# Optimization experiments

Hardware: AMD Instinct MI355X
Metric: run time of the kernel (lower is better)

## Reference

```python
import jax, jax.numpy as jnp
import numpy as np

# Scattering config (matches init_kwargs)
J, L, MAX_ORDER = 3, 8, 2
H = W = 128
LEN_COEFF = 1 + J * L + L * L * (J * (J - 1) // 2)  # 217
B = 16
N_OUT = 6


def _gabor_2d(M, N, sigma, theta, xi, slant):
    """Periodized 2D Gabor centered at (0,0), kymatio convention."""
    R = np.array([[np.cos(theta), -np.sin(theta)], [np.sin(theta), np.cos(theta)]])
    D = np.array([[1.0, 0.0], [0.0, slant * slant]])
    curv = R @ D @ R.T / (2.0 * sigma * sigma)
    gab = np.zeros((M, N), np.complex128)
    for ex in range(-2, 3):
        for ey in range(-2, 3):
            xx, yy = np.mgrid[ex * M:(ex + 1) * M, ey * N:(ey + 1) * N]
            arg = -(curv[0, 0] * xx * xx + (curv[0, 1] + curv[1, 0]) * xx * yy
                    + curv[1, 1] * yy * yy) \
                  + 1j * xi * (xx * np.cos(theta) + yy * np.sin(theta))
            gab += np.exp(arg)
    return gab / (2.0 * np.pi * sigma * sigma / slant)


def _morlet_2d(M, N, sigma, theta, xi, slant):
    wv = _gabor_2d(M, N, sigma, theta, xi, slant)
    g = _gabor_2d(M, N, sigma, theta, 0.0, slant)
    K = wv.sum() / g.sum()  # zero-mean correction
    return wv - K * g


def _filter_bank(M, N, J_, L_):
    psi = np.zeros((J_, L_, M, N), np.complex64)
    for j in range(J_):
        sigma = 0.8 * 2.0 ** j
        xi = 3.0 / 4.0 * np.pi / 2.0 ** j
        for l in range(L_):
            theta = (int(L_ - L_ / 2 - 1) - l) * np.pi / L_
            psi[j, l] = np.fft.fft2(
                _morlet_2d(M, N, sigma, theta, xi, 4.0 / L_)).astype(np.complex64)
    phi = np.fft.fft2(
        _gabor_2d(M, N, 0.8 * 2.0 ** (J_ - 1), 0.0, 0.0, 1.0)).astype(np.complex64)
    return jnp.asarray(phi), jnp.asarray(psi)


def setup_inputs() -> dict:
    key = jax.random.key(0)
    k1, k2, k3 = jax.random.split(key, 3)
    x = jax.random.normal(k1, (B, H, W), dtype=jnp.float32)
    weight = jax.random.normal(k2, (N_OUT, LEN_COEFF), dtype=jnp.float32) / np.sqrt(LEN_COEFF)
    bias = jax.random.normal(k3, (N_OUT,), dtype=jnp.float32) * 0.01
    phi_f, psi_f = _filter_bank(H, W, J, L)
    return {"x": x, "weight": weight, "bias": bias, "phi_f": phi_f, "psi_f": psi_f}


def _scattering(x, phi_f, psi_f):
    # x: (B,H,W); phi_f: (H,W) complex; psi_f: (J,L,H,W) complex (Fourier-domain)
    k = 2 ** J
    xf = jnp.fft.fft2(x)
    # Order 0: low-pass then subsample by 2^J (exact spatial subsample of band-limited conv)
    outs = [jnp.fft.ifft2(xf * phi_f).real[:, None, ::k, ::k]]  # (B,1,h,w)
    U1 = []
    for j1 in range(J):
        u1 = jnp.abs(jnp.fft.ifft2(xf[:, None] * psi_f[j1]))  # (B,L,H,W)
        U1.append(u1)
        outs.append(jnp.fft.ifft2(jnp.fft.fft2(u1) * phi_f).real[..., ::k, ::k])
    if MAX_ORDER >= 2:
        for j1 in range(J):
            u1f = jnp.fft.fft2(U1[j1])  # (B,L,H,W)
            for j2 in range(j1 + 1, J):
                u2 = jnp.abs(jnp.fft.ifft2(u1f[:, :, None] * psi_f[j2]))  # (B,L,L,H,W)
                s2 = jnp.fft.ifft2(jnp.fft.fft2(u2) * phi_f).real[..., ::k, ::k]
                outs.append(s2.reshape(s2.shape[0], L * L, H // k, W // k))
    return jnp.concatenate(outs, axis=1)  # (B, LEN_COEFF, h, w)


def reference(x, weight, bias, phi_f, psi_f):
    coeffs = _scattering(x, phi_f, psi_f)            # (B, 217, 16, 16)
    coeffs_spav = coeffs.mean(axis=(-2, -1))         # spatial average -> (B, 217)
    out = coeffs_spav @ weight.T + bias              # Linear(217 -> 6)
    return out                                       # Identity output activation
```

## Files before the change

kernel.cpp:

```cpp
#include <hip/hip_runtime.h>
#include <math.h>


#define HW 128
#define NPIX 16384
#define NCOEFF 217
#define NB 16
#define NOUT 6
#define NT 1024
#define NBLK2 3072
#define PI_F 3.14159265358979f
#define CMAX_EPS 1e-6f

__device__ float  g_w8[64];
__device__ float  g_psi[24 * NPIX];
__device__ float  g_cmax[24 * 128];
__device__ float  g_coeffs[NB * NCOEFF];
__device__ unsigned g_ticket;
__device__ float2 g_xf[NB * NPIX];
__device__ float  g_u1[NB * 16 * NPIX];
__device__ float2 g_u1f[NB * 16 * NPIX];

#if defined(__has_builtin)
#  if __has_builtin(__builtin_amdgcn_permlane32_swap)
#    define USE_PL32 1
#  else
#    define USE_PL32 0
#  endif
#  if __has_builtin(__builtin_amdgcn_permlane16_swap)
#    define USE_PL16 1
#  else
#    define USE_PL16 0
#  endif
#else
#  define USE_PL32 0
#  define USE_PL16 0
#endif

__device__ __forceinline__ float2 cmul2(float2 a, float2 b) {
  return make_float2(a.x*b.x - a.y*b.y, a.x*b.y + a.y*b.x);
}
__device__ __forceinline__ float2 cmulc2(float2 a, float2 b) {
  return make_float2(a.x*b.x + a.y*b.y, a.y*b.x - a.x*b.y);
}
__device__ __forceinline__ float fsqrt_fast(float x) {
  return __builtin_amdgcn_sqrtf(x);
}

template <int S>
__device__ __forceinline__ float shx(float v) {
  if constexpr (S == 1)
    return __int_as_float(__builtin_amdgcn_mov_dpp(
        __float_as_int(v), 0xB1, 0xF, 0xF, true));
  else if constexpr (S == 2)
    return __int_as_float(__builtin_amdgcn_mov_dpp(
        __float_as_int(v), 0x4E, 0xF, 0xF, true));
  else if constexpr (S == 4)
    return __int_as_float(__builtin_amdgcn_ds_swizzle(
        __float_as_int(v), 0x101F));
  else if constexpr (S == 8)
    return __int_as_float(__builtin_amdgcn_mov_dpp(
        __float_as_int(v), 0x128, 0xF, 0xF, true));
  else
    return __shfl_xor(v, S);
}

__device__ __forceinline__ float bft32(float v, float sg) {
#if USE_PL32
  auto r = __builtin_amdgcn_permlane32_swap(
      __float_as_int(v), __float_as_int(v), false, false);
  return fmaf(sg, __int_as_float(r[1]), __int_as_float(r[0]));
#else
  return fmaf(sg, v, __shfl_xor(v, 32));
#endif
}
__device__ __forceinline__ float bft16(float v, float sg) {
#if USE_PL16
  auto r = __builtin_amdgcn_permlane16_swap(
      __float_as_int(v), __float_as_int(v), false, false);
  return fmaf(sg, __int_as_float(r[1]), __int_as_float(r[0]));
#else
  return fmaf(sg, v, __shfl_xor(v, 16));
#endif
}

__device__ __forceinline__ float2 cndrot_n(float2 u, bool m) {
  return m ? make_float2(u.y, -u.x) : u;
}
__device__ __forceinline__ float2 cndrot_p(float2 u, bool m) {
  return m ? make_float2(-u.y, u.x) : u;
}

struct TwState {
  float2 tw0, wA, wB;
  float  sg[6];
  bool   rA, rB, rC;
};

__device__ __forceinline__ void make_tw(int lane, TwState &T) {
  float s, c;
  sincosf(-PI_F * (float)lane / 64.f, &s, &c);
  T.tw0 = make_float2(c, s);
  int kA = 2 * ((lane >> 4) & 1) + ((lane >> 5) & 1);
  sincosf(-PI_F * (float)((lane & 15) * kA) / 32.f, &s, &c);
  T.wA = make_float2(c, s);
  int kB = 2 * ((lane >> 2) & 1) + ((lane >> 3) & 1);
  sincosf(-PI_F * (float)((lane & 3) * kB) / 8.f, &s, &c);
  T.wB = make_float2(c, s);
#pragma unroll
  for (int k = 0; k < 6; ++k)
    T.sg[k] = (lane & (32 >> k)) ? -1.f : 1.f;
  T.rA = (lane & 48) == 48;
  T.rB = (lane & 12) == 12;
  T.rC = (lane & 3) == 3;
}

__device__ __forceinline__ float2 fwd_p32(float2 v, const TwState &T) {
  float2 u; u.x = bft32(v.x, T.sg[0]); u.y = bft32(v.y, T.sg[0]);
  u = cndrot_n(u, T.rA);
  float2 t; t.x = bft16(u.x, T.sg[1]); t.y = bft16(u.y, T.sg[1]);
  return cmul2(t, T.wA);
}
__device__ __forceinline__ float2 fwd_p8(float2 v, const TwState &T) {
  float2 u; u.x = fmaf(T.sg[2], v.x, shx<8>(v.x));
            u.y = fmaf(T.sg[2], v.y, shx<8>(v.y));
  u = cndrot_n(u, T.rB);
  float2 t; t.x = fmaf(T.sg[3], u.x, shx<4>(u.x));
            t.y = fmaf(T.sg[3], u.y, shx<4>(u.y));
  return cmul2(t, T.wB);
}
__device__ __forceinline__ float2 fwd_p2(float2 v, const TwState &T) {
  float2 u; u.x = fmaf(T.sg[4], v.x, shx<2>(v.x));
            u.y = fmaf(T.sg[4], v.y, shx<2>(v.y));
  u = cndrot_n(u, T.rC);
  float2 t; t.x = fmaf(T.sg[5], u.x, shx<1>(u.x));
            t.y = fmaf(T.sg[5], u.y, shx<1>(u.y));
  return t;
}
__device__ __forceinline__ float2 inv_p1(float2 v, const TwState &T) {
  float2 u; u.x = fmaf(T.sg[5], v.x, shx<1>(v.x));
            u.y = fmaf(T.sg[5], v.y, shx<1>(v.y));
  u = cndrot_p(u, T.rC);
  float2 t; t.x = fmaf(T.sg[4], u.x, shx<2>(u.x));
            t.y = fmaf(T.sg[4], u.y, shx<2>(u.y));
  return t;
}
__device__ __forceinline__ float2 inv_p4(float2 v, const TwState &T) {
  float2 m = cmulc2(v, T.wB);
  float2 u; u.x = fmaf(T.sg[3], m.x, shx<4>(m.x));
            u.y = fmaf(T.sg[3], m.y, shx<4>(m.y));
  u = cndrot_p(u, T.rB);
  float2 t; t.x = fmaf(T.sg[2], u.x, shx<8>(u.x));
            t.y = fmaf(T.sg[2], u.y, shx<8>(u.y));
  return t;
}
__device__ __forceinline__ float2 inv_p16(float2 v, const TwState &T) {
  float2 m = cmulc2(v, T.wA);
  float2 u; u.x = bft16(m.x, T.sg[1]); u.y = bft16(m.y, T.sg[1]);
  u = cndrot_p(u, T.rA);
  float2 t; t.x = bft32(u.x, T.sg[0]); t.y = bft32(u.y, T.sg[0]);
  return t;
}

__device__ __forceinline__ void fft128_fwd(float2 &a, float2 &b, const TwState &T) {
  float2 t = make_float2(a.x - b.x, a.y - b.y);
  a = make_float2(a.x + b.x, a.y + b.y);
  b = cmul2(t, T.tw0);
  a = fwd_p32(a, T); b = fwd_p32(b, T);
  a = fwd_p8(a, T);  b = fwd_p8(b, T);
  a = fwd_p2(a, T);  b = fwd_p2(b, T);
}

__device__ __forceinline__ void fft128_inv(float2 &a, float2 &b, const TwState &T) {
  a = inv_p1(a, T);  b = inv_p1(b, T);
  a = inv_p4(a, T);  b = inv_p4(b, T);
  a = inv_p16(a, T); b = inv_p16(b, T);
  float2 t = cmulc2(b, T.tw0);
  float2 na = make_float2(a.x + t.x, a.y + t.y);
  b = make_float2(a.x - t.x, a.y - t.y);
  a = na;
}

__device__ __forceinline__ int fmap(int p) {
  int l = p & 63, t = p >> 6;
  int br = (int)(__brev((unsigned)l) >> 26);
  return 2 * br + t;
}

__device__ __forceinline__ void fparams(int f, float &sig, float &xi, float &co, float &si) {
  int j = f >> 3, l = f & 7;
  sig = 0.8f * (float)(1 << j);
  xi = 0.75f * PI_F / (float)(1 << j);
  float th = (float)(3 - l) * PI_F / 8.f;
  sincosf(th, &si, &co);
}

__device__ __forceinline__ float gab_hat_fast(float tr, float tc, float sig,
                                              float xi, float co, float si, int j) {
  float hs = 0.5f * sig * sig;
  int m1lo, m1hi, m2lo, m2hi;
  if (j == 0)      { m1lo = -1; m1hi = 1; m2lo = -1; m2hi = 1; }
  else if (j == 1) { m1lo = -1; m1hi = 0; m2lo = -1; m2hi = 0; }
  else {
    m1lo = (tr > 0.5f) ? -1 : 0; m1hi = m1lo;
    m2lo = (tc > 0.5f) ? -1 : 0; m2hi = m2lo;
  }
  float acc = 0.f;
  for (int m1 = m1lo; m1 <= m1hi; ++m1)
    for (int m2 = m2lo; m2 <= m2hi; ++m2) {
      float w1 = 2.f * PI_F * (tr + (float)m1) - xi * co;
      float w2 = 2.f * PI_F * (tc + (float)m2) - xi * si;
      float a1 = co * w1 + si * w2;
      float a2 = -si * w1 + co * w2;
      acc += __expf(-hs * (a1 * a1 + 4.f * a2 * a2));
    }
  return acc;
}

__device__ __forceinline__ float ct8(int k) {
  k &= 7;
  float m = (k & 1) ? 0.70710678118654752f : ((k & 2) ? 0.f : 1.f);
  return (k >= 3 && k <= 5) ? -m : m;
}

__device__ __forceinline__ void transp(const float2 va[8], const float2 vb[8],
                                       float2 na[8], float2 nb[8],
                                       int w, int l, float2* buf) {
#pragma unroll
  for (int i = 0; i < 8; ++i) buf[(w + 16 * i) * 65 + l] = va[i];
  __syncthreads();
#pragma unroll
  for (int k = 0; k < 4; ++k) {
    na[k] = buf[l * 65 + 16 * k + w];
    nb[k] = buf[(l + 64) * 65 + 16 * k + w];
  }
  __syncthreads();
#pragma unroll
  for (int i = 0; i < 8; ++i) buf[(w + 16 * i) * 65 + l] = vb[i];
  __syncthreads();
#pragma unroll
  for (int k = 0; k < 4; ++k) {
    na[4 + k] = buf[l * 65 + 16 * k + w];
    nb[4 + k] = buf[(l + 64) * 65 + 16 * k + w];
  }
}

__global__ void __launch_bounds__(NT, 4)
k_prep(const float* __restrict__ x) {
  __shared__ float2 buf[128 * 65];
  __shared__ float red[16];
  __shared__ float w8s[64];
  __shared__ float sK[2];
  int tid = threadIdx.x, blk = blockIdx.x;
  if (blk >= NB) {
    if (blk == NB && tid == 0) g_ticket = 0;
    int idx = (blk - NB) * NT + tid;
    int f = idx >> 14;
    int q = idx & (NPIX - 1);
    int pc = q >> 7, pr = q & 127;
    float tr = (float)fmap(pr) / 128.f;
    float tc = (float)fmap(pc) / 128.f;
    float sig, xi, co, si;
    fparams(f, sig, xi, co, si);
    int j = f >> 3;
    float hsK = 0.5f * sig * sig;
    int wv = tid >> 6;
    if (wv < 2) {
      int t = tid & 63;
      float term = 0.f;
      if (t < 25) {
        int m1 = t / 5 - 2, m2 = t % 5 - 2;
        float xe = (wv == 0) ? xi : 0.f;
        float w1 = 2.f * PI_F * (float)m1 - xe * co;
        float w2 = 2.f * PI_F * (float)m2 - xe * si;
        float a1 = co * w1 + si * w2, a2 = -si * w1 + co * w2;
        term = expf(-hsK * (a1 * a1 + 4.f * a2 * a2));
      }
      for (int off = 32; off; off >>= 1) term += __shfl_xor(term, off);
      if (t == 0) sK[wv] = term;
    }
    __syncthreads();
    float Kf = sK[0] / sK[1];
    float p = gab_hat_fast(tr, tc, sig, xi, co, si, j)
            - Kf * gab_hat_fast(tr, tc, sig, 0.f, co, si, j);
    g_psi[idx] = p;
    float m = fabsf(p);
    for (int off = 32; off; off >>= 1) m = fmaxf(m, __shfl_xor(m, off));
    if ((tid & 63) == 0)
      atomicMax((unsigned int*)&g_cmax[idx >> 7], __float_as_uint(m));
    return;
  }
  int b = blk;
  int l = tid & 63, w = tid >> 6;
  if (tid < 64) {
    const float hs8 = 0.5f * 3.2f * 3.2f;
    float P[8];
#pragma unroll
    for (int K = 0; K < 8; ++K) {
      float acc = 0.f;
      for (int m = -2; m <= 2; ++m) {
        float wv = 2.f * PI_F * ((float)K / 8.f + (float)m);
        acc += expf(-hs8 * wv * wv);
      }
      P[K] = acc;
    }
    int r = tid >> 3, s = tid & 7;
    float acc = 0.f;
#pragma unroll
    for (int K1 = 0; K1 < 8; ++K1)
#pragma unroll
      for (int K2 = 0; K2 < 8; ++K2)
        acc += P[K1] * P[K2] * ct8(K1 * r + K2 * s);
    w8s[tid] = acc;
    g_w8[tid] = acc;
  }
  TwState T; make_tw(l, T);
  const float inv = 1.f / 16384.f;
  const float* xb = x + b * NPIX;
  float2 va[8], vb[8], na[8], nb[8];
  float sacc = 0.f;
#pragma unroll
  for (int i = 0; i < 8; ++i) {
    int r = w + 16 * i;
    float v0 = xb[r * HW + l], v1 = xb[r * HW + l + 64];
    va[i] = make_float2(v0, 0.f); vb[i] = make_float2(v1, 0.f);
    sacc += v0 + v1;
  }
  __syncthreads();
  float w8v = w8s[((w & 7) << 3) | (l & 7)];
  sacc *= w8v;
  for (int off = 32; off; off >>= 1) sacc += __shfl_xor(sacc, off);
  if (l == 0) red[w] = sacc;
#pragma unroll
  for (int i = 0; i < 8; ++i) fft128_fwd(va[i], vb[i], T);
  transp(va, vb, na, nb, w, l, buf);
#pragma unroll
  for (int j = 0; j < 8; ++j) fft128_fwd(na[j], nb[j], T);
  float2* o = g_xf + (size_t)b * NPIX;
#pragma unroll
  for (int j = 0; j < 8; ++j) {
    int c = w + 16 * j;
    o[c * HW + l] = na[j];
    o[c * HW + l + 64] = nb[j];
  }
  if (tid == 0) {
    float s = 0.f;
    for (int i = 0; i < 16; ++i) s += red[i];
    g_coeffs[b * NCOEFF + 0] = s * inv;
  }
}

__global__ void __launch_bounds__(NT, 4)
k_inv1() {
  __shared__ float2 buf[128 * 65];
  __shared__ float red[16];
  __shared__ float w8s[64];
  int tid = threadIdx.x, blk = blockIdx.x;
  int b = blk / 24, f = blk % 24;
  int l = tid & 63, w = tid >> 6;
  if (tid < 64) w8s[tid] = g_w8[tid];
  TwState T; make_tw(l, T);
  const float inv = 1.f / 16384.f;
  const float2* X = g_xf + (size_t)b * NPIX;
  const float*  P = g_psi + f * NPIX;
  float2 va[8], vb[8], na[8], nb[8];
  bool kp[8];
#pragma unroll
  for (int j = 0; j < 8; ++j) {
    int c = w + 16 * j;
    kp[j] = g_cmax[f * 128 + c] > CMAX_EPS;
    if (kp[j]) {
      float2 x0 = X[c * HW + l], x1 = X[c * HW + l + 64];
      float p0 = P[c * HW + l],  p1 = P[c * HW + l + 64];
      na[j] = make_float2(x0.x * p0, x0.y * p0);
      nb[j] = make_float2(x1.x * p1, x1.y * p1);
    } else {
      na[j] = make_float2(0.f, 0.f);
      nb[j] = make_float2(0.f, 0.f);
    }
  }
#pragma unroll
  for (int j = 0; j < 8; ++j) if (kp[j]) fft128_inv(na[j], nb[j], T);
  transp(na, nb, va, vb, w, l, buf);
#pragma unroll
  for (int i = 0; i < 8; ++i) fft128_inv(va[i], vb[i], T);
  float w8v = w8s[((w & 7) << 3) | (l & 7)];
  float s1 = 0.f;
  float u0a[8], u1a[8];
#pragma unroll
  for (int i = 0; i < 8; ++i) {
    u0a[i] = fsqrt_fast(va[i].x * va[i].x + va[i].y * va[i].y);
    u1a[i] = fsqrt_fast(vb[i].x * vb[i].x + vb[i].y * vb[i].y);
    s1 += u0a[i] + u1a[i];
  }
  s1 *= w8v;
  for (int off = 32; off; off >>= 1) s1 += __shfl_xor(s1, off);
  if (l == 0) red[w] = s1;
  __syncthreads();
  if (tid == 0) {
    float s = 0.f;
    for (int i = 0; i < 16; ++i) s += red[i];
    g_coeffs[b * NCOEFF + 1 + f] = s * (inv * inv);
  }
  if (f < 16) {
    float* o = g_u1 + (size_t)(b * 16 + f) * NPIX;
#pragma unroll
    for (int i = 0; i < 8; ++i) {
      int r = w + 16 * i;
      o[r * HW + l] = u0a[i];
      o[r * HW + l + 64] = u1a[i];
    }
  }
}

__global__ void __launch_bounds__(NT, 4)
k_fwd1() {
  __shared__ float2 buf[128 * 65];
  int tid = threadIdx.x, chan = blockIdx.x;
  int l = tid & 63, w = tid >> 6;
  TwState T; make_tw(l, T);
  const float* u = g_u1 + (size_t)chan * NPIX;
  float2 va[8], vb[8], na[8], nb[8];
#pragma unroll
  for (int i = 0; i < 8; ++i) {
    int r = w + 16 * i;
    va[i] = make_float2(u[r * HW + l], 0.f);
    vb[i] = make_float2(u[r * HW + l + 64], 0.f);
  }
#pragma unroll
  for (int i = 0; i < 8; ++i) fft128_fwd(va[i], vb[i], T);
  transp(va, vb, na, nb, w, l, buf);
#pragma unroll
  for (int j = 0; j < 8; ++j) fft128_fwd(na[j], nb[j], T);
  float2* o = g_u1f + (size_t)chan * NPIX;
#pragma unroll
  for (int j = 0; j < 8; ++j) {
    int c = w + 16 * j;
    o[c * HW + l] = na[j];
    o[c * HW + l + 64] = nb[j];
  }
}

__global__ void __launch_bounds__(NT, 4)
k_order2(const float* __restrict__ wgt, const float* __restrict__ bias,
         float* __restrict__ out) {
  __shared__ float2 buf[128 * 65];
  __shared__ float red[16];
  __shared__ float w8s[64];
  __shared__ unsigned sLast;
  int tid = threadIdx.x, blk = blockIdx.x;
  int b, pair, l1, l2, j1, j2;
  if (blk < 2048) {
    l1 = blk & 7;
    int t = blk >> 3;
    b = t >> 4;
    int cons = t & 15;
    pair = cons >> 3;
    j2 = 1 + pair;
    l2 = cons & 7;
    j1 = 0;
  } else {
    int rr = blk - 2048;
    l1 = rr & 7;
    int t = rr >> 3;
    b = t >> 3;
    l2 = t & 7;
    j1 = 1; j2 = 2; pair = 2;
  }
  int fi = j2 * 8 + l2;
  int l = tid & 63, w = tid >> 6;
  if (tid < 64) w8s[tid] = g_w8[tid];
  TwState T; make_tw(l, T);
  const float inv = 1.f / 16384.f;
  const float2* X = g_u1f + (size_t)(b * 16 + j1 * 8 + l1) * NPIX;
  const float*  P = g_psi + fi * NPIX;
  float2 va[8], vb[8], na[8], nb[8];
  bool kp[8];
#pragma unroll
  for (int j = 0; j < 8; ++j) {
    int c = w + 16 * j;
    kp[j] = g_cmax[fi * 128 + c] > CMAX_EPS;
    if (kp[j]) {
      float2 x0 = X[c * HW + l], x1 = X[c * HW + l + 64];
      float p0 = P[c * HW + l],  p1 = P[c * HW + l + 64];
      na[j] = make_float2(x0.x * p0, x0.y * p0);
      nb[j] = make_float2(x1.x * p1, x1.y * p1);
    } else {
      na[j] = make_float2(0.f, 0.f);
      nb[j] = make_float2(0.f, 0.f);
    }
  }
#pragma unroll
  for (int j = 0; j < 8; ++j) if (kp[j]) fft128_inv(na[j], nb[j], T);
  transp(na, nb, va, vb, w, l, buf);
#pragma unroll
  for (int i = 0; i < 8; ++i) fft128_inv(va[i], vb[i], T);
  float w8v = w8s[((w & 7) << 3) | (l & 7)];
  float s2 = 0.f;
#pragma unroll
  for (int i = 0; i < 8; ++i) {
    s2 += fsqrt_fast(va[i].x * va[i].x + va[i].y * va[i].y);
    s2 += fsqrt_fast(vb[i].x * vb[i].x + vb[i].y * vb[i].y);
  }
  s2 *= (inv * inv) * w8v;
  for (int off = 32; off; off >>= 1) s2 += __shfl_xor(s2, off);
  if (l == 0) red[w] = s2;
  __syncthreads();
  if (tid == 0) {
    float s = 0.f;
    for (int i = 0; i < 16; ++i) s += red[i];
    g_coeffs[b * NCOEFF + 25 + pair * 64 + l1 * 8 + l2] = s * inv;
    __threadfence();
    unsigned old = atomicAdd(&g_ticket, 1u);
    sLast = (old == NBLK2 - 1) ? 1u : 0u;
  }
  __syncthreads();
  if (sLast) {
    __threadfence();
    if (tid < NB * NOUT) {
      int bb = tid / NOUT, o = tid % NOUT;
      float s = bias[o];
      for (int c = 0; c < NCOEFF; ++c)
        s += g_coeffs[bb * NCOEFF + c] * wgt[o * NCOEFF + c];
      out[tid] = s;
    }
  }
}

extern "C" void kernel_launch(void* const* d_in, const int* in_sizes, int n_in,
                              void* d_out, int out_size, void* d_ws, size_t ws_size,
                              hipStream_t stream) {
  const float* x    = (const float*)d_in[0];
  const float* wgt  = (const float*)d_in[1];
  const float* bias = (const float*)d_in[2];
  float* out = (float*)d_out;
  (void)d_ws; (void)ws_size; (void)in_sizes; (void)n_in; (void)out_size;

  k_prep<<<NB + 384, NT, 0, stream>>>(x);
  k_inv1<<<NB * 24, NT, 0, stream>>>();
  k_fwd1<<<NB * 16, NT, 0, stream>>>();
  k_order2<<<NBLK2, NT, 0, stream>>>(wgt, bias, out);
}
```

Measured before the change: 286.8 us.

## Fuse forward FFT of U1 into inverse kernel and split final linear out

The forward 2D FFT of first-order modulus maps now runs directly in k_inv1 on register-resident values, so the g_u1 intermediate buffer and the separate k_fwd1 launch go away. This removes a global round trip of the U1 real maps and one kernel launch. The atomic ticket and last-block reduction in k_order2 are replaced by a small separate k_linear kernel, which drops the per-block fence and atomic but adds a launch. The fused kernel may need more registers and shared-memory work per block, which can lower occupancy in k_inv1.

```diff
diff --git a/kernel.cpp b/kernel.cpp
--- a/kernel.cpp
+++ b/kernel.cpp
@@ -16,9 +16,7 @@
 __device__ float  g_psi[24 * NPIX];
 __device__ float  g_cmax[24 * 128];
 __device__ float  g_coeffs[NB * NCOEFF];
-__device__ unsigned g_ticket;
 __device__ float2 g_xf[NB * NPIX];
-__device__ float  g_u1[NB * 16 * NPIX];
 __device__ float2 g_u1f[NB * 16 * NPIX];
 
 #if defined(__has_builtin)
@@ -253,7 +251,6 @@
   __shared__ float sK[2];
   int tid = threadIdx.x, blk = blockIdx.x;
   if (blk >= NB) {
-    if (blk == NB && tid == 0) g_ticket = 0;
     int idx = (blk - NB) * NT + tid;
     int f = idx >> 14;
     int q = idx & (NPIX - 1);
@@ -403,51 +400,31 @@
     g_coeffs[b * NCOEFF + 1 + f] = s * (inv * inv);
   }
   if (f < 16) {
-    float* o = g_u1 + (size_t)(b * 16 + f) * NPIX;
 #pragma unroll
     for (int i = 0; i < 8; ++i) {
-      int r = w + 16 * i;
-      o[r * HW + l] = u0a[i];
-      o[r * HW + l + 64] = u1a[i];
+      va[i] = make_float2(u0a[i], 0.f);
+      vb[i] = make_float2(u1a[i], 0.f);
+    }
+#pragma unroll
+    for (int i = 0; i < 8; ++i) fft128_fwd(va[i], vb[i], T);
+    transp(va, vb, na, nb, w, l, buf);
+#pragma unroll
+    for (int j = 0; j < 8; ++j) fft128_fwd(na[j], nb[j], T);
+    float2* o = g_u1f + (size_t)(b * 16 + f) * NPIX;
+#pragma unroll
+    for (int j = 0; j < 8; ++j) {
+      int c = w + 16 * j;
+      o[c * HW + l] = na[j];
+      o[c * HW + l + 64] = nb[j];
     }
   }
 }
 
 __global__ void __launch_bounds__(NT, 4)
-k_fwd1() {
-  __shared__ float2 buf[128 * 65];
-  int tid = threadIdx.x, chan = blockIdx.x;
-  int l = tid & 63, w = tid >> 6;
-  TwState T; make_tw(l, T);
-  const float* u = g_u1 + (size_t)chan * NPIX;
-  float2 va[8], vb[8], na[8], nb[8];
-#pragma unroll
-  for (int i = 0; i < 8; ++i) {
-    int r = w + 16 * i;
-    va[i] = make_float2(u[r * HW + l], 0.f);
-    vb[i] = make_float2(u[r * HW + l + 64], 0.f);
-  }
-#pragma unroll
-  for (int i = 0; i < 8; ++i) fft128_fwd(va[i], vb[i], T);
-  transp(va, vb, na, nb, w, l, buf);
-#pragma unroll
-  for (int j = 0; j < 8; ++j) fft128_fwd(na[j], nb[j], T);
-  float2* o = g_u1f + (size_t)chan * NPIX;
-#pragma unroll
-  for (int j = 0; j < 8; ++j) {
-    int c = w + 16 * j;
-    o[c * HW + l] = na[j];
-    o[c * HW + l + 64] = nb[j];
-  }
-}
-
-__global__ void __launch_bounds__(NT, 4)
-k_order2(const float* __restrict__ wgt, const float* __restrict__ bias,
-         float* __restrict__ out) {
+k_order2() {
   __shared__ float2 buf[128 * 65];
   __shared__ float red[16];
   __shared__ float w8s[64];
-  __shared__ unsigned sLast;
   int tid = threadIdx.x, blk = blockIdx.x;
   int b, pair, l1, l2, j1, j2;
   if (blk < 2048) {
@@ -510,21 +487,19 @@
     float s = 0.f;
     for (int i = 0; i < 16; ++i) s += red[i];
     g_coeffs[b * NCOEFF + 25 + pair * 64 + l1 * 8 + l2] = s * inv;
-    __threadfence();
-    unsigned old = atomicAdd(&g_ticket, 1u);
-    sLast = (old == NBLK2 - 1) ? 1u : 0u;
-  }
-  __syncthreads();
-  if (sLast) {
-    __threadfence();
-    if (tid < NB * NOUT) {
-      int bb = tid / NOUT, o = tid % NOUT;
-      float s = bias[o];
-      for (int c = 0; c < NCOEFF; ++c)
-        s += g_coeffs[bb * NCOEFF + c] * wgt[o * NCOEFF + c];
-      out[tid] = s;
-    }
-  }
+  }
+}
+
+__global__ void k_linear(const float* __restrict__ wgt,
+                         const float* __restrict__ bias,
+                         float* __restrict__ out) {
+  int t = threadIdx.x;
+  if (t >= NB * NOUT) return;
+  int b = t / NOUT, o = t % NOUT;
+  float s = bias[o];
+  for (int c = 0; c < NCOEFF; ++c)
+    s += g_coeffs[b * NCOEFF + c] * wgt[o * NCOEFF + c];
+  out[t] = s;
 }
 
 extern "C" void kernel_launch(void* const* d_in, const int* in_sizes, int n_in,
@@ -538,6 +513,6 @@
 
   k_prep<<<NB + 384, NT, 0, stream>>>(x);
   k_inv1<<<NB * 24, NT, 0, stream>>>();
-  k_fwd1<<<NB * 16, NT, 0, stream>>>();
-  k_order2<<<NBLK2, NT, 0, stream>>>(wgt, bias, out);
-}
+  k_order2<<<NBLK2, NT, 0, stream>>>();
+  k_linear<<<1, 128, 0, stream>>>(wgt, bias, out);
+}
```

New measurement: 282.8 us. Within noise of the previous version (-1.4%).
